# Kernel optimization log

Hardware: AMD Instinct MI355X
Metric: run time of the kernel (lower is better)

The kernel has to match this reference:

```python
import jax, jax.numpy as jnp
import numpy as np

NEG_INF = -1e30


def setup_inputs() -> dict:
    key = jax.random.key(0)
    ks = jax.random.split(key, 8)
    B, T, d, H = 4, 1024, 512, 8
    scale = 1.0 / np.sqrt(d)
    return {
        "self_seq": jax.random.normal(ks[0], (B, T, d), jnp.float32),
        "cross_seq": jax.random.normal(ks[1], (B, T, d), jnp.float32),
        "self_seq_time": jax.random.randint(ks[2], (B, T), 0, 100000, jnp.int64 if jax.config.jax_enable_x64 else jnp.int32),
        "cross_seq_time": jax.random.randint(ks[3], (B, T), 0, 100000, jnp.int64 if jax.config.jax_enable_x64 else jnp.int32),
        "W_self": jax.random.normal(ks[4], (d, 3 * d), jnp.float32) * scale,
        "b_self": jnp.zeros((3 * d,), jnp.float32),
        "W_cross": jax.random.normal(ks[5], (d, 3 * d), jnp.float32) * scale,
        "b_cross": jnp.zeros((3 * d,), jnp.float32),
        "W_proj": jax.random.normal(ks[6], (d, d), jnp.float32) * scale,
        "b_proj": jnp.zeros((d,), jnp.float32),
    }


def _split_heads(x, H):
    B, T, d = x.shape
    return x.reshape(B, T, H, d // H).transpose(0, 2, 1, 3)  # (B,H,T,hd)


def reference(self_seq, cross_seq, self_seq_time, cross_seq_time,
              W_self, b_self, W_cross, b_cross, W_proj, b_proj):
    B, T_s, d = self_seq.shape
    T_c = cross_seq.shape[1]
    H = 8
    hd = d // H

    qkv_s = self_seq @ W_self + b_self          # (B,Ts,3d)
    q_s, k_s, v_s = jnp.split(qkv_s, 3, axis=2)
    qkv_c = cross_seq @ W_cross + b_cross       # (B,Tc,3d)
    q_c, k_c, v_c = jnp.split(qkv_c, 3, axis=2)

    q = jnp.concatenate([_split_heads(q_s, H), _split_heads(q_c, H)], axis=2)  # (B,H,T,hd)
    k = jnp.concatenate([_split_heads(k_s, H), _split_heads(k_c, H)], axis=2)
    v = jnp.concatenate([_split_heads(v_s, H), _split_heads(v_c, H)], axis=2)

    t = jnp.concatenate([self_seq_time, cross_seq_time], axis=1)  # (B,T)
    mask = (t[:, None, :, None] >= t[:, None, None, :])           # (B,1,T,T)

    scores = jnp.einsum("bhqd,bhkd->bhqk", q, k) * (1.0 / np.sqrt(hd))
    scores = jnp.where(mask, scores, NEG_INF)
    att = jax.nn.softmax(scores, axis=-1)
    y = jnp.einsum("bhqk,bhkd->bhqd", att, v)                     # (B,H,T,hd)

    Ttot = T_s + T_c
    y = y.transpose(0, 2, 1, 3).reshape(B, Ttot, d)
    y = y @ W_proj + b_proj
    return (y[:, :T_s], y[:, T_s:])
```

## Files before the change

kernel.cpp:

```cpp
#include <hip/hip_runtime.h>


typedef short     bf16x8 __attribute__((ext_vector_type(8)));
typedef short     bf16x4 __attribute__((ext_vector_type(4)));
typedef float     f32x4  __attribute__((ext_vector_type(4)));
typedef int       i32x4  __attribute__((ext_vector_type(4)));

#define DI __device__ __forceinline__

DI unsigned short f2b(float f) {
    union { float f; unsigned int u; } x; x.f = f;
    unsigned int r = x.u + 0x7fffu + ((x.u >> 16) & 1u);
    return (unsigned short)(r >> 16);
}
DI unsigned int fbits(float f) { union { float f; unsigned int u; } x; x.f = f; return x.u; }
DI float bitsf(unsigned int u) { union { unsigned int u; float f; } x; x.u = u; return x.f; }
DI float b2f(unsigned short v) { return bitsf(((unsigned int)v) << 16); }

DI void glds16(const unsigned short* g, unsigned short* l) {
    __builtin_amdgcn_global_load_lds(
        (const __attribute__((address_space(1))) void*)g,
        (__attribute__((address_space(3))) void*)l, 16, 0, 0);
}
DI void glds16i(const int* g, int* l) {
    __builtin_amdgcn_global_load_lds(
        (const __attribute__((address_space(1))) void*)g,
        (__attribute__((address_space(3))) void*)l, 16, 0, 0);
}

#define QSCALE 0.18033688011112042f

__global__ __launch_bounds__(256)
void prep_kernel(const float* __restrict__ Xs, const float* __restrict__ Xc,
                 const float* __restrict__ Ws, const float* __restrict__ Wc,
                 const float* __restrict__ Wp,
                 unsigned short* __restrict__ xb, unsigned short* __restrict__ wt,
                 unsigned short* __restrict__ wtp)
{
    const int bid = blockIdx.x, tid = threadIdx.x;
    if (bid < 2048) {
        int idx = bid * 2048 + tid * 8;
        const float* s = (idx < 2097152) ? (Xs + idx) : (Xc + idx - 2097152);
        f32x4 a0 = *(const f32x4*)s;
        f32x4 a1 = *(const f32x4*)(s + 4);
        bf16x8 v;
#pragma unroll
        for (int j = 0; j < 4; ++j) {
            ((unsigned short*)&v)[j]     = f2b(a0[j]);
            ((unsigned short*)&v)[4 + j] = f2b(a1[j]);
        }
        *(bf16x8*)(xb + idx) = v;
        return;
    }
    __shared__ unsigned short Tt[64 * 72];
    const float* W;
    unsigned short* dst;
    int k0, n0, ldn;
    float sc = 1.0f;
    if (bid < 2432) {
        int tj  = bid - 2048;
        int src = tj >= 192;  tj -= src * 192;
        k0  = (tj / 24) * 64;
        n0  = (tj % 24) * 64;
        W   = src ? Wc : Ws;
        ldn = 1536;
        dst = wt + (size_t)src * 786432;
        if (n0 < 512) sc = QSCALE;
    } else {
        int tj = bid - 2432;
        k0  = (tj >> 3) * 64;
        n0  = (tj & 7) * 64;
        W   = Wp;
        ldn = 512;
        dst = wtp;
    }
#pragma unroll
    for (int r = 0; r < 4; ++r) {
        int g  = tid + r * 256;
        int kr = g >> 4, nc4 = (g & 15) * 4;
        f32x4 v = *(const f32x4*)(W + (size_t)(k0 + kr) * ldn + n0 + nc4);
#pragma unroll
        for (int u = 0; u < 4; ++u)
            Tt[(nc4 + u) * 72 + kr] = f2b(v[u] * sc);
    }
    __syncthreads();
#pragma unroll
    for (int r = 0; r < 2; ++r) {
        int c = tid + r * 256;
        int nl = c >> 3, k8 = (c & 7) * 8;
        *(bf16x8*)(dst + (size_t)(n0 + nl) * 512 + k0 + k8) =
            *(const bf16x8*)(Tt + nl * 72 + k8);
    }
}

__global__ __launch_bounds__(256)
void qkv_kernel(const unsigned short* __restrict__ xb,
                const unsigned short* __restrict__ wt,
                const float* __restrict__ bs, const float* __restrict__ bc,
                unsigned short* __restrict__ qb, unsigned short* __restrict__ kb,
                unsigned short* __restrict__ vtb)
{
    const int src = blockIdx.z;
    const int m0 = blockIdx.x * 128, n0 = blockIdx.y * 128;
    const float* bias = src ? bc : bs;
    const unsigned short* X = xb + (size_t)src * 2097152;
    const unsigned short* W = wt + (size_t)src * 786432;

    __shared__ unsigned short As[128 * 32];
    __shared__ unsigned short Bs[128 * 32];

    const int tid = threadIdx.x, lane = tid & 63, w = tid >> 6;
    const int quad = lane >> 4, r16 = lane & 15;
    const int mrow = (w >> 1) * 64, ncol = (w & 1) * 64;

    const f32x4 fz = {0.f, 0.f, 0.f, 0.f};
    f32x4 acc[4][4];
#pragma unroll
    for (int a = 0; a < 4; ++a)
#pragma unroll
        for (int b = 0; b < 4; ++b) acc[a][b] = fz;

    const int ci   = w << 1;
    const int rofs = lane >> 2, kofs = (lane & 3) * 8;
    const unsigned short* gA = X + (size_t)(m0 + ci * 16 + rofs) * 512 + kofs;
    const unsigned short* gB = W + (size_t)(n0 + ci * 16 + rofs) * 512 + kofs;
    unsigned short* lA = As + ci * 512 + lane * 8;
    unsigned short* lB = Bs + ci * 512 + lane * 8;

    for (int k0 = 0; k0 < 512; k0 += 32) {
        glds16(gA + k0, lA);
        glds16(gA + 16 * 512 + k0, lA + 512);
        glds16(gB + k0, lB);
        glds16(gB + 16 * 512 + k0, lB + 512);
        __syncthreads();

        bf16x8 af[4], bfr[4];
#pragma unroll
        for (int ms = 0; ms < 4; ++ms)
            af[ms] = *(const bf16x8*)(As + (mrow + ms * 16 + r16) * 32 + quad * 8);
#pragma unroll
        for (int ns = 0; ns < 4; ++ns)
            bfr[ns] = *(const bf16x8*)(Bs + (ncol + ns * 16 + r16) * 32 + quad * 8);
#pragma unroll
        for (int ms = 0; ms < 4; ++ms)
#pragma unroll
            for (int ns = 0; ns < 4; ++ns)
                acc[ms][ns] = __builtin_amdgcn_mfma_f32_16x16x32_bf16(
                    af[ms], bfr[ns], acc[ms][ns], 0, 0, 0);
        __syncthreads();
    }

#pragma unroll
    for (int ms = 0; ms < 4; ++ms)
#pragma unroll
        for (int ns = 0; ns < 4; ++ns) {
            int n = n0 + ncol + ns * 16 + r16;
            int sec = n >> 9, col = n & 511;
            int hh = col >> 6, j = col & 63;
            float bb = bias[n] * ((sec == 0) ? QSCALE : 1.0f);
            int mb = m0 + mrow + ms * 16 + quad * 4;
            int bi = mb >> 10, tg0 = (mb & 1023) + (src << 10);
            if (sec == 2) {
                bf16x4 pk;
#pragma unroll
                for (int i = 0; i < 4; ++i)
                    pk[i] = (short)f2b(acc[ms][ns][i] + bb);
                int r = tg0 & 31;
                int pos = (r < 16) ? (r << 1) : (((r - 16) << 1) + 4);
                int tgp = (tg0 & ~31) + pos;
                *(bf16x4*)(vtb + (((size_t)(bi * 8 + hh) * 64 + j) << 11) + tgp) = pk;
            } else {
                unsigned short* dst = (sec == 0) ? qb : kb;
#pragma unroll
                for (int i = 0; i < 4; ++i)
                    dst[(((size_t)(bi * 8 + hh) * 2048 + tg0 + i) << 6) + j] =
                        f2b(acc[ms][ns][i] + bb);
            }
        }
}


#define STAGE(BB, T) do {                                                      \
    _Pragma("unroll")                                                          \
    for (int r_ = 0; r_ < 2; ++r_) {                                           \
        const int j_ = (w << 1) + r_;                                          \
        const int row_ = (j_ << 3) + rofs;                                     \
        glds16(Kg + (size_t)(((T) << 6) + row_) * 64 + lsw,                    \
               &Kl[BB][(j_ << 9) + lane * 8]);                                 \
        glds16(Vg + (size_t)row_ * 2048 + ((T) << 6) + lsw,                    \
               &Vl[BB][(j_ << 9) + lane * 8]);                                 \
    }                                                                          \
} while (0)

#define DOG(G, TQ, PF) do {                                                    \
    f32x4 s0_ = fz, s1_ = fz;                                                  \
    __builtin_amdgcn_s_setprio(1);                                             \
    s0_ = __builtin_amdgcn_mfma_f32_16x16x32_bf16(ka00, qf[G][0], s0_, 0, 0, 0); \
    s0_ = __builtin_amdgcn_mfma_f32_16x16x32_bf16(ka01, qf[G][1], s0_, 0, 0, 0); \
    s1_ = __builtin_amdgcn_mfma_f32_16x16x32_bf16(ka10, qf[G][0], s1_, 0, 0, 0); \
    s1_ = __builtin_amdgcn_mfma_f32_16x16x32_bf16(ka11, qf[G][1], s1_, 0, 0, 0); \
    __builtin_amdgcn_s_setprio(0);                                             \
    float e_[8];                                                               \
    _Pragma("unroll")                                                          \
    for (int i_ = 0; i_ < 4; ++i_) {                                           \
        float a0_ = ((TQ) >= tk0[i_]) ? s0_[i_] : -1e9f;                       \
        float a1_ = ((TQ) >= tk1[i_]) ? s1_[i_] : -1e9f;                       \
        e_[i_]     = __builtin_amdgcn_exp2f(a0_);                              \
        e_[4 + i_] = __builtin_amdgcn_exp2f(a1_);                              \
    }                                                                          \
    union { unsigned int d[4]; bf16x8 v; } pu_;                                \
    pu_.d[0] = __builtin_amdgcn_perm(fbits(e_[1]), fbits(e_[0]), 0x07060302u); \
    pu_.d[1] = __builtin_amdgcn_perm(fbits(e_[3]), fbits(e_[2]), 0x07060302u); \
    pu_.d[2] = __builtin_amdgcn_perm(fbits(e_[5]), fbits(e_[4]), 0x07060302u); \
    pu_.d[3] = __builtin_amdgcn_perm(fbits(e_[7]), fbits(e_[6]), 0x07060302u); \
    PF = pu_.v;                                                                \
    al[G] = __builtin_amdgcn_mfma_f32_16x16x32_bf16(ones, PF, al[G], 0, 0, 0); \
} while (0)

#define DOTILE(BB, T) do {                                                     \
    const unsigned short* Kb_ = Kl[BB];                                        \
    const unsigned short* Vb_ = Vl[BB];                                        \
    _Pragma("unroll")                                                          \
    for (int c_ = 0; c_ < 2; ++c_) {                                           \
        bf16x8 ka00 = *(const bf16x8*)(Kb_ + (c_ * 32 + r16) * 64 + ((quad ^ rsx) << 3));        \
        bf16x8 ka01 = *(const bf16x8*)(Kb_ + (c_ * 32 + r16) * 64 + (((quad + 4) ^ rsx) << 3));  \
        bf16x8 ka10 = *(const bf16x8*)(Kb_ + (c_ * 32 + 16 + r16) * 64 + ((quad ^ rsx) << 3));   \
        bf16x8 ka11 = *(const bf16x8*)(Kb_ + (c_ * 32 + 16 + r16) * 64 + (((quad + 4) ^ rsx) << 3)); \
        i32x4 tk0 = *(const i32x4*)(Ts + ((T) << 6) + c_ * 32 + quad * 4);     \
        i32x4 tk1 = *(const i32x4*)(Ts + ((T) << 6) + c_ * 32 + 16 + quad * 4);\
        const int vs_ = ((4 * c_ + quad) ^ rsx) << 3;                          \
        bf16x8 va0 = *(const bf16x8*)(Vb_ + (r16) * 64 + vs_);                 \
        bf16x8 va1 = *(const bf16x8*)(Vb_ + (16 + r16) * 64 + vs_);            \
        bf16x8 va2 = *(const bf16x8*)(Vb_ + (32 + r16) * 64 + vs_);            \
        bf16x8 va3 = *(const bf16x8*)(Vb_ + (48 + r16) * 64 + vs_);            \
        bf16x8 pf0, pf1;                                                       \
        DOG(0, tq0, pf0);                                                      \
        DOG(1, tq1, pf1);                                                      \
        __builtin_amdgcn_s_setprio(1);                                         \
        ot[0][0] = __builtin_amdgcn_mfma_f32_16x16x32_bf16(va0, pf0, ot[0][0], 0, 0, 0); \
        ot[1][0] = __builtin_amdgcn_mfma_f32_16x16x32_bf16(va0, pf1, ot[1][0], 0, 0, 0); \
        ot[0][1] = __builtin_amdgcn_mfma_f32_16x16x32_bf16(va1, pf0, ot[0][1], 0, 0, 0); \
        ot[1][1] = __builtin_amdgcn_mfma_f32_16x16x32_bf16(va1, pf1, ot[1][1], 0, 0, 0); \
        ot[0][2] = __builtin_amdgcn_mfma_f32_16x16x32_bf16(va2, pf0, ot[0][2], 0, 0, 0); \
        ot[1][2] = __builtin_amdgcn_mfma_f32_16x16x32_bf16(va2, pf1, ot[1][2], 0, 0, 0); \
        ot[0][3] = __builtin_amdgcn_mfma_f32_16x16x32_bf16(va3, pf0, ot[0][3], 0, 0, 0); \
        ot[1][3] = __builtin_amdgcn_mfma_f32_16x16x32_bf16(va3, pf1, ot[1][3], 0, 0, 0); \
        __builtin_amdgcn_s_setprio(0);                                         \
    }                                                                          \
} while (0)

__global__ __launch_bounds__(256, 2)
void attn_kernel(const unsigned short* __restrict__ qb,
                 const unsigned short* __restrict__ kb,
                 const unsigned short* __restrict__ vt,
                 const int* __restrict__ t_self, const int* __restrict__ t_cross,
                 unsigned short* __restrict__ y)
{
    const int bid = blockIdx.x;
    const int bh = ((bid & 7) << 2) | ((bid >> 3) & 3);
    const int qt = bid >> 5;
    const int b = bh >> 3, h = bh & 7;
    const int tid = threadIdx.x, w = tid >> 6, lane = tid & 63;
    const int quad = lane >> 4, r16 = lane & 15;
    const int rofs = lane >> 3;
    const int lsw  = ((lane & 7) ^ rofs) << 3;
    const int rsx  = r16 & 7;

    const unsigned short* Q  = qb + (size_t)bh * 131072;
    const unsigned short* Kg = kb + (size_t)bh * 131072;
    const unsigned short* Vg = vt + (size_t)bh * 131072;
    const int* tsb = t_self + b * 1024;
    const int* tcb = t_cross + b * 1024;

    __shared__ unsigned short Kl[2][4096];
    __shared__ unsigned short Vl[2][4096];
    __shared__ int Ts[2048];

#pragma unroll
    for (int r = 0; r < 2; ++r) {
        const int sg = (w << 1) + r;
        const int* src = (sg < 4) ? (tsb + sg * 256) : (tcb + (sg - 4) * 256);
        glds16i(src + lane * 4, Ts + sg * 256 + lane * 4);
    }

    const int q0w = qt * 128 + w * 32;
    bf16x8 qf[2][2];
#pragma unroll
    for (int g = 0; g < 2; ++g)
#pragma unroll
        for (int ks = 0; ks < 2; ++ks)
            qf[g][ks] = *(const bf16x8*)(Q + (size_t)(q0w + g * 16 + r16) * 64
                                           + ks * 32 + quad * 8);
    const int* tqp = (q0w < 1024) ? (tsb + q0w) : (tcb + (q0w - 1024));
    const int tq0 = tqp[r16];
    const int tq1 = tqp[16 + r16];

    const f32x4 fz = {0.f, 0.f, 0.f, 0.f};
    f32x4 ot[2][4], al[2];
#pragma unroll
    for (int g = 0; g < 2; ++g) {
        al[g] = fz;
#pragma unroll
        for (int nt = 0; nt < 4; ++nt) ot[g][nt] = fz;
    }
    const bf16x8 ones = {(short)0x3F80, (short)0x3F80, (short)0x3F80, (short)0x3F80,
                         (short)0x3F80, (short)0x3F80, (short)0x3F80, (short)0x3F80};

    STAGE(0, 0);
    __syncthreads();

    for (int T = 0; T < 32; T += 2) {
        STAGE(1, T + 1);
        DOTILE(0, T);
        __syncthreads();
        if (T + 2 < 32) STAGE(0, T + 2);
        DOTILE(1, T + 1);
        __syncthreads();
    }

#pragma unroll
    for (int g = 0; g < 2; ++g) {
        const float l = al[g][0];
        const float inv = (l > 0.f) ? (1.f / l) : 0.f;
        const size_t base = (((size_t)(b * 2048 + q0w + g * 16 + r16)) << 9) + h * 64;
#pragma unroll
        for (int nt = 0; nt < 4; ++nt) {
            bf16x4 pk;
#pragma unroll
            for (int i = 0; i < 4; ++i) pk[i] = (short)f2b(ot[g][nt][i] * inv);
            *(bf16x4*)(y + base + nt * 16 + quad * 4) = pk;
        }
    }
}

#undef STAGE
#undef DOG
#undef DOTILE

__global__ __launch_bounds__(256)
void proj_kernel(const unsigned short* __restrict__ X,
                 const unsigned short* __restrict__ Wt,
                 const float* __restrict__ bias,
                 float* __restrict__ out)
{
    const int m0 = blockIdx.x * 128, n0 = blockIdx.y * 128;
    __shared__ unsigned short As[128 * 32];
    __shared__ unsigned short Bs[128 * 32];

    const int tid = threadIdx.x, lane = tid & 63, w = tid >> 6;
    const int quad = lane >> 4, r16 = lane & 15;
    const int mrow = (w >> 1) * 64, ncol = (w & 1) * 64;

    const f32x4 fz = {0.f, 0.f, 0.f, 0.f};
    f32x4 acc[4][4];
#pragma unroll
    for (int a = 0; a < 4; ++a)
#pragma unroll
        for (int b = 0; b < 4; ++b) acc[a][b] = fz;

    const int ci   = w << 1;
    const int rofs = lane >> 2, kofs = (lane & 3) * 8;
    const unsigned short* gA = X + (size_t)(m0 + ci * 16 + rofs) * 512 + kofs;
    const unsigned short* gB = Wt + (size_t)(n0 + ci * 16 + rofs) * 512 + kofs;
    unsigned short* lA = As + ci * 512 + lane * 8;
    unsigned short* lB = Bs + ci * 512 + lane * 8;

    for (int k0 = 0; k0 < 512; k0 += 32) {
        glds16(gA + k0, lA);
        glds16(gA + 16 * 512 + k0, lA + 512);
        glds16(gB + k0, lB);
        glds16(gB + 16 * 512 + k0, lB + 512);
        __syncthreads();

        bf16x8 af[4], bfr[4];
#pragma unroll
        for (int ms = 0; ms < 4; ++ms)
            af[ms] = *(const bf16x8*)(As + (mrow + ms * 16 + r16) * 32 + quad * 8);
#pragma unroll
        for (int ns = 0; ns < 4; ++ns)
            bfr[ns] = *(const bf16x8*)(Bs + (ncol + ns * 16 + r16) * 32 + quad * 8);
#pragma unroll
        for (int ms = 0; ms < 4; ++ms)
#pragma unroll
            for (int ns = 0; ns < 4; ++ns)
                acc[ms][ns] = __builtin_amdgcn_mfma_f32_16x16x32_bf16(
                    af[ms], bfr[ns], acc[ms][ns], 0, 0, 0);
        __syncthreads();
    }

#pragma unroll
    for (int ms = 0; ms < 4; ++ms)
#pragma unroll
        for (int ns = 0; ns < 4; ++ns) {
            int n = n0 + ncol + ns * 16 + r16;
            float bb = bias[n];
#pragma unroll
            for (int i = 0; i < 4; ++i) {
                int m = m0 + mrow + ms * 16 + quad * 4 + i;
                int bi = m >> 11, t = m & 2047;
                float v = acc[ms][ns][i] + bb;
                size_t idx = (t < 1024)
                    ? ((size_t)bi * 1024 + t) * 512 + n
                    : (size_t)2097152 + ((size_t)bi * 1024 + (t - 1024)) * 512 + n;
                out[idx] = v;
            }
        }
}

extern "C" void kernel_launch(void* const* d_in, const int* in_sizes, int n_in,
                              void* d_out, int out_size, void* d_ws, size_t ws_size,
                              hipStream_t stream)
{
    const float* self_seq  = (const float*)d_in[0];
    const float* cross_seq = (const float*)d_in[1];
    const int*   t_self    = (const int*)d_in[2];
    const int*   t_cross   = (const int*)d_in[3];
    const float* W_self    = (const float*)d_in[4];
    const float* b_self    = (const float*)d_in[5];
    const float* W_cross   = (const float*)d_in[6];
    const float* b_cross   = (const float*)d_in[7];
    const float* W_proj    = (const float*)d_in[8];
    const float* b_proj    = (const float*)d_in[9];
    float* out = (float*)d_out;

    unsigned short* qbuf = (unsigned short*)d_ws;
    unsigned short* kbuf = qbuf + 4194304;
    unsigned short* vtb  = kbuf + 4194304;
    unsigned short* ybuf = vtb + 4194304;
    unsigned short* xb   = (unsigned short*)d_out;
    unsigned short* wt   = xb + 4194304;
    unsigned short* wtp  = wt + 1572864;

    prep_kernel<<<dim3(2496), 256, 0, stream>>>(
        self_seq, cross_seq, W_self, W_cross, W_proj, xb, wt, wtp);

    qkv_kernel<<<dim3(32, 12, 2), 256, 0, stream>>>(
        xb, wt, b_self, b_cross, qbuf, kbuf, vtb);

    attn_kernel<<<dim3(512), 256, 0, stream>>>(
        qbuf, kbuf, vtb, t_self, t_cross, ybuf);

    proj_kernel<<<dim3(64, 4), 256, 0, stream>>>(
        ybuf, wtp, b_proj, out);
}
```

Baseline: 178.0 us.

## Halve attention and projection tiles per block to raise occupancy and grid size

The attention kernel now processes 16 query rows per wave (64 per block) instead of 32, doubling the grid to 1024 blocks and raising the launch-bounds occupancy hint to 4 blocks per CU. Key timestamps are now streamed per tile into a small double-buffered LDS array alongside K/V instead of preloading all 2048 into shared memory, which shrinks LDS use. The projection GEMM tile shrinks from 128x128 to 64x128, doubling its grid. The intent is better latency hiding and CU fill, at the cost of reloading K/V tiles twice as often per query and less MFMA work per LDS read.

```diff
diff --git a/kernel.cpp b/kernel.cpp
--- a/kernel.cpp
+++ b/kernel.cpp
@@ -190,21 +190,25 @@
         glds16(Vg + (size_t)row_ * 2048 + ((T) << 6) + lsw,                    \
                &Vl[BB][(j_ << 9) + lane * 8]);                                 \
     }                                                                          \
+    if (w == 3 && lane < 16) {                                                 \
+        const int* tt_ = ((T) < 16) ? (tsb + ((T) << 6)) : (tcb + (((T) - 16) << 6)); \
+        glds16i(tt_ + lane * 4, &Tl[BB][lane * 4]);                            \
+    }                                                                          \
 } while (0)
 
-#define DOG(G, TQ, PF) do {                                                    \
+#define DOG(PF) do {                                                           \
     f32x4 s0_ = fz, s1_ = fz;                                                  \
     __builtin_amdgcn_s_setprio(1);                                             \
-    s0_ = __builtin_amdgcn_mfma_f32_16x16x32_bf16(ka00, qf[G][0], s0_, 0, 0, 0); \
-    s0_ = __builtin_amdgcn_mfma_f32_16x16x32_bf16(ka01, qf[G][1], s0_, 0, 0, 0); \
-    s1_ = __builtin_amdgcn_mfma_f32_16x16x32_bf16(ka10, qf[G][0], s1_, 0, 0, 0); \
-    s1_ = __builtin_amdgcn_mfma_f32_16x16x32_bf16(ka11, qf[G][1], s1_, 0, 0, 0); \
+    s0_ = __builtin_amdgcn_mfma_f32_16x16x32_bf16(ka00, qf[0], s0_, 0, 0, 0);  \
+    s0_ = __builtin_amdgcn_mfma_f32_16x16x32_bf16(ka01, qf[1], s0_, 0, 0, 0);  \
+    s1_ = __builtin_amdgcn_mfma_f32_16x16x32_bf16(ka10, qf[0], s1_, 0, 0, 0);  \
+    s1_ = __builtin_amdgcn_mfma_f32_16x16x32_bf16(ka11, qf[1], s1_, 0, 0, 0);  \
     __builtin_amdgcn_s_setprio(0);                                             \
     float e_[8];                                                               \
     _Pragma("unroll")                                                          \
     for (int i_ = 0; i_ < 4; ++i_) {                                           \
-        float a0_ = ((TQ) >= tk0[i_]) ? s0_[i_] : -1e9f;                       \
-        float a1_ = ((TQ) >= tk1[i_]) ? s1_[i_] : -1e9f;                       \
+        float a0_ = (tq0 >= tk0[i_]) ? s0_[i_] : -1e9f;                        \
+        float a1_ = (tq0 >= tk1[i_]) ? s1_[i_] : -1e9f;                        \
         e_[i_]     = __builtin_amdgcn_exp2f(a0_);                              \
         e_[4 + i_] = __builtin_amdgcn_exp2f(a1_);                              \
     }                                                                          \
@@ -214,10 +218,10 @@
     pu_.d[2] = __builtin_amdgcn_perm(fbits(e_[5]), fbits(e_[4]), 0x07060302u); \
     pu_.d[3] = __builtin_amdgcn_perm(fbits(e_[7]), fbits(e_[6]), 0x07060302u); \
     PF = pu_.v;                                                                \
-    al[G] = __builtin_amdgcn_mfma_f32_16x16x32_bf16(ones, PF, al[G], 0, 0, 0); \
+    al = __builtin_amdgcn_mfma_f32_16x16x32_bf16(ones, PF, al, 0, 0, 0);       \
 } while (0)
 
-#define DOTILE(BB, T) do {                                                     \
+#define DOTILE(BB) do {                                                        \
     const unsigned short* Kb_ = Kl[BB];                                        \
     const unsigned short* Vb_ = Vl[BB];                                        \
     _Pragma("unroll")                                                          \
@@ -226,30 +230,25 @@
         bf16x8 ka01 = *(const bf16x8*)(Kb_ + (c_ * 32 + r16) * 64 + (((quad + 4) ^ rsx) << 3));  \
         bf16x8 ka10 = *(const bf16x8*)(Kb_ + (c_ * 32 + 16 + r16) * 64 + ((quad ^ rsx) << 3));   \
         bf16x8 ka11 = *(const bf16x8*)(Kb_ + (c_ * 32 + 16 + r16) * 64 + (((quad + 4) ^ rsx) << 3)); \
-        i32x4 tk0 = *(const i32x4*)(Ts + ((T) << 6) + c_ * 32 + quad * 4);     \
-        i32x4 tk1 = *(const i32x4*)(Ts + ((T) << 6) + c_ * 32 + 16 + quad * 4);\
+        i32x4 tk0 = *(const i32x4*)(Tl[BB] + c_ * 32 + quad * 4);              \
+        i32x4 tk1 = *(const i32x4*)(Tl[BB] + c_ * 32 + 16 + quad * 4);         \
         const int vs_ = ((4 * c_ + quad) ^ rsx) << 3;                          \
         bf16x8 va0 = *(const bf16x8*)(Vb_ + (r16) * 64 + vs_);                 \
         bf16x8 va1 = *(const bf16x8*)(Vb_ + (16 + r16) * 64 + vs_);            \
         bf16x8 va2 = *(const bf16x8*)(Vb_ + (32 + r16) * 64 + vs_);            \
         bf16x8 va3 = *(const bf16x8*)(Vb_ + (48 + r16) * 64 + vs_);            \
-        bf16x8 pf0, pf1;                                                       \
-        DOG(0, tq0, pf0);                                                      \
-        DOG(1, tq1, pf1);                                                      \
+        bf16x8 pf;                                                             \
+        DOG(pf);                                                               \
         __builtin_amdgcn_s_setprio(1);                                         \
-        ot[0][0] = __builtin_amdgcn_mfma_f32_16x16x32_bf16(va0, pf0, ot[0][0], 0, 0, 0); \
-        ot[1][0] = __builtin_amdgcn_mfma_f32_16x16x32_bf16(va0, pf1, ot[1][0], 0, 0, 0); \
-        ot[0][1] = __builtin_amdgcn_mfma_f32_16x16x32_bf16(va1, pf0, ot[0][1], 0, 0, 0); \
-        ot[1][1] = __builtin_amdgcn_mfma_f32_16x16x32_bf16(va1, pf1, ot[1][1], 0, 0, 0); \
-        ot[0][2] = __builtin_amdgcn_mfma_f32_16x16x32_bf16(va2, pf0, ot[0][2], 0, 0, 0); \
-        ot[1][2] = __builtin_amdgcn_mfma_f32_16x16x32_bf16(va2, pf1, ot[1][2], 0, 0, 0); \
-        ot[0][3] = __builtin_amdgcn_mfma_f32_16x16x32_bf16(va3, pf0, ot[0][3], 0, 0, 0); \
-        ot[1][3] = __builtin_amdgcn_mfma_f32_16x16x32_bf16(va3, pf1, ot[1][3], 0, 0, 0); \
+        ot[0] = __builtin_amdgcn_mfma_f32_16x16x32_bf16(va0, pf, ot[0], 0, 0, 0); \
+        ot[1] = __builtin_amdgcn_mfma_f32_16x16x32_bf16(va1, pf, ot[1], 0, 0, 0); \
+        ot[2] = __builtin_amdgcn_mfma_f32_16x16x32_bf16(va2, pf, ot[2], 0, 0, 0); \
+        ot[3] = __builtin_amdgcn_mfma_f32_16x16x32_bf16(va3, pf, ot[3], 0, 0, 0); \
         __builtin_amdgcn_s_setprio(0);                                         \
     }                                                                          \
 } while (0)
 
-__global__ __launch_bounds__(256, 2)
+__global__ __launch_bounds__(256, 4)
 void attn_kernel(const unsigned short* __restrict__ qb,
                  const unsigned short* __restrict__ kb,
                  const unsigned short* __restrict__ vt,
@@ -274,35 +273,21 @@
 
     __shared__ unsigned short Kl[2][4096];
     __shared__ unsigned short Vl[2][4096];
-    __shared__ int Ts[2048];
-
-#pragma unroll
-    for (int r = 0; r < 2; ++r) {
-        const int sg = (w << 1) + r;
-        const int* src = (sg < 4) ? (tsb + sg * 256) : (tcb + (sg - 4) * 256);
-        glds16i(src + lane * 4, Ts + sg * 256 + lane * 4);
-    }
-
-    const int q0w = qt * 128 + w * 32;
-    bf16x8 qf[2][2];
-#pragma unroll
-    for (int g = 0; g < 2; ++g)
-#pragma unroll
-        for (int ks = 0; ks < 2; ++ks)
-            qf[g][ks] = *(const bf16x8*)(Q + (size_t)(q0w + g * 16 + r16) * 64
-                                           + ks * 32 + quad * 8);
+    __shared__ __align__(16) int Tl[2][64];
+
+    const int q0w = qt * 64 + w * 16;
+    bf16x8 qf[2];
+#pragma unroll
+    for (int ks = 0; ks < 2; ++ks)
+        qf[ks] = *(const bf16x8*)(Q + (size_t)(q0w + r16) * 64 + ks * 32 + quad * 8);
     const int* tqp = (q0w < 1024) ? (tsb + q0w) : (tcb + (q0w - 1024));
     const int tq0 = tqp[r16];
-    const int tq1 = tqp[16 + r16];
 
     const f32x4 fz = {0.f, 0.f, 0.f, 0.f};
-    f32x4 ot[2][4], al[2];
-#pragma unroll
-    for (int g = 0; g < 2; ++g) {
-        al[g] = fz;
-#pragma unroll
-        for (int nt = 0; nt < 4; ++nt) ot[g][nt] = fz;
-    }
+    f32x4 ot[4], al;
+    al = fz;
+#pragma unroll
+    for (int nt = 0; nt < 4; ++nt) ot[nt] = fz;
     const bf16x8 ones = {(short)0x3F80, (short)0x3F80, (short)0x3F80, (short)0x3F80,
                          (short)0x3F80, (short)0x3F80, (short)0x3F80, (short)0x3F80};
 
@@ -311,23 +296,22 @@
 
     for (int T = 0; T < 32; T += 2) {
         STAGE(1, T + 1);
-        DOTILE(0, T);
+        DOTILE(0);
         __syncthreads();
         if (T + 2 < 32) STAGE(0, T + 2);
-        DOTILE(1, T + 1);
-        __syncthreads();
-    }
-
-#pragma unroll
-    for (int g = 0; g < 2; ++g) {
-        const float l = al[g][0];
+        DOTILE(1);
+        __syncthreads();
+    }
+
+    {
+        const float l = al[0];
         const float inv = (l > 0.f) ? (1.f / l) : 0.f;
-        const size_t base = (((size_t)(b * 2048 + q0w + g * 16 + r16)) << 9) + h * 64;
+        const size_t base = (((size_t)(b * 2048 + q0w + r16)) << 9) + h * 64;
 #pragma unroll
         for (int nt = 0; nt < 4; ++nt) {
             bf16x4 pk;
 #pragma unroll
-            for (int i = 0; i < 4; ++i) pk[i] = (short)f2b(ot[g][nt][i] * inv);
+            for (int i = 0; i < 4; ++i) pk[i] = (short)f2b(ot[nt][i] * inv);
             *(bf16x4*)(y + base + nt * 16 + quad * 4) = pk;
         }
     }
@@ -343,44 +327,42 @@
                  const float* __restrict__ bias,
                  float* __restrict__ out)
 {
-    const int m0 = blockIdx.x * 128, n0 = blockIdx.y * 128;
-    __shared__ unsigned short As[128 * 32];
+    const int m0 = blockIdx.x * 64, n0 = blockIdx.y * 128;
+    __shared__ unsigned short As[64 * 32];
     __shared__ unsigned short Bs[128 * 32];
 
     const int tid = threadIdx.x, lane = tid & 63, w = tid >> 6;
     const int quad = lane >> 4, r16 = lane & 15;
-    const int mrow = (w >> 1) * 64, ncol = (w & 1) * 64;
+    const int mrow = (w >> 1) * 32, ncol = (w & 1) * 64;
 
     const f32x4 fz = {0.f, 0.f, 0.f, 0.f};
-    f32x4 acc[4][4];
-#pragma unroll
-    for (int a = 0; a < 4; ++a)
+    f32x4 acc[2][4];
+#pragma unroll
+    for (int a = 0; a < 2; ++a)
 #pragma unroll
         for (int b = 0; b < 4; ++b) acc[a][b] = fz;
 
-    const int ci   = w << 1;
     const int rofs = lane >> 2, kofs = (lane & 3) * 8;
-    const unsigned short* gA = X + (size_t)(m0 + ci * 16 + rofs) * 512 + kofs;
-    const unsigned short* gB = Wt + (size_t)(n0 + ci * 16 + rofs) * 512 + kofs;
-    unsigned short* lA = As + ci * 512 + lane * 8;
-    unsigned short* lB = Bs + ci * 512 + lane * 8;
+    const unsigned short* gA = X + (size_t)(m0 + w * 16 + rofs) * 512 + kofs;
+    const unsigned short* gB = Wt + (size_t)(n0 + (w << 1) * 16 + rofs) * 512 + kofs;
+    unsigned short* lA = As + w * 512 + lane * 8;
+    unsigned short* lB = Bs + (w << 1) * 512 + lane * 8;
 
     for (int k0 = 0; k0 < 512; k0 += 32) {
         glds16(gA + k0, lA);
-        glds16(gA + 16 * 512 + k0, lA + 512);
         glds16(gB + k0, lB);
         glds16(gB + 16 * 512 + k0, lB + 512);
         __syncthreads();
 
-        bf16x8 af[4], bfr[4];
-#pragma unroll
-        for (int ms = 0; ms < 4; ++ms)
+        bf16x8 af[2], bfr[4];
+#pragma unroll
+        for (int ms = 0; ms < 2; ++ms)
             af[ms] = *(const bf16x8*)(As + (mrow + ms * 16 + r16) * 32 + quad * 8);
 #pragma unroll
         for (int ns = 0; ns < 4; ++ns)
             bfr[ns] = *(const bf16x8*)(Bs + (ncol + ns * 16 + r16) * 32 + quad * 8);
 #pragma unroll
-        for (int ms = 0; ms < 4; ++ms)
+        for (int ms = 0; ms < 2; ++ms)
 #pragma unroll
             for (int ns = 0; ns < 4; ++ns)
                 acc[ms][ns] = __builtin_amdgcn_mfma_f32_16x16x32_bf16(
@@ -389,7 +371,7 @@
     }
 
 #pragma unroll
-    for (int ms = 0; ms < 4; ++ms)
+    for (int ms = 0; ms < 2; ++ms)
 #pragma unroll
         for (int ns = 0; ns < 4; ++ns) {
             int n = n0 + ncol + ns * 16 + r16;
@@ -437,9 +419,9 @@
     qkv_kernel<<<dim3(32, 12, 2), 256, 0, stream>>>(
         xb, wt, b_self, b_cross, qbuf, kbuf, vtb);
 
-    attn_kernel<<<dim3(512), 256, 0, stream>>>(
+    attn_kernel<<<dim3(1024), 256, 0, stream>>>(
         qbuf, kbuf, vtb, t_self, t_cross, ybuf);
 
-    proj_kernel<<<dim3(64, 4), 256, 0, stream>>>(
+    proj_kernel<<<dim3(128, 4), 256, 0, stream>>>(
         ybuf, wtp, b_proj, out);
 }
```

Measured after the change: 175.9 us. Within noise of the previous version (-1.2%).
